# Performance work log

Hardware: AMD Instinct MI355X
Metric: run time of the kernel (lower is better)

## Reference

```python
import jax, jax.numpy as jnp
import numpy as np

B, C, H, W = 1, 128, 384, 512
MAX_DISP = 3  # 7x7 = 49 shifts


def setup_inputs() -> dict:
    key = jax.random.key(0)
    kx, ky = jax.random.split(key)
    x = jax.random.normal(kx, (B, C, H, W), dtype=jnp.float32)
    y = jax.random.normal(ky, (B, C, H, W), dtype=jnp.float32)
    return {"x": x, "y": y}


def reference(x, y):
    # out[j*7+i, h, w] = sum_{b,c} x[b,c,h,w] * y[b,c,h+(j-3), w+(i-3)]
    # with zero padding for out-of-range y (exactly the torch pad/slice math).
    b, c, h, w = x.shape
    yp = jnp.pad(y, ((0, 0), (0, 0), (MAX_DISP, MAX_DISP), (MAX_DISP, MAX_DISP)))
    outs = []
    for j in range(2 * MAX_DISP + 1):      # shiftY = j - 3
        for i in range(2 * MAX_DISP + 1):  # shiftX = i - 3
            # start (pad + shiftY, pad + shiftX) = (j, i)
            ysh = jax.lax.dynamic_slice(yp, (0, 0, j, i), (b, c, h, w))
            outs.append(jnp.sum(x * ysh, axis=(0, 1)))  # sum over batch AND channel
    out = jnp.stack(outs)           # [49, H, W]
    return out[None]                # [1, 49, H, W]
```

## Files before the change

### kernel.cpp

```cpp
#include <hip/hip_runtime.h>
#include <stdint.h>


typedef __attribute__((ext_vector_type(8))) short short8;
typedef __attribute__((ext_vector_type(4))) float floatx4;

constexpr int C = 128;
constexpr int H = 384;
constexpr int W = 512;
constexpr int HW = H * W;

constexpr int NROW = 10;
constexpr int NCOL = 40;
constexpr int KP   = 40;
constexpr int ROWB = NCOL * KP * 2;
constexpr int BUFE = NROW * NCOL * KP;
constexpr int NUNIT = NROW * 4 * (NCOL / 2);

__device__ __forceinline__ uint32_t pkbf(float a, float b) {
  uint32_t ua = (__float_as_uint(a) + 0x8000u) >> 16;
  uint32_t ub = (__float_as_uint(b) + 0x8000u) & 0xffff0000u;
  return ua | ub;
}

union S8U { uint32_t u[4]; short8 s; };

__device__ __forceinline__ void stage_unit(const float* __restrict__ y,
                                           uint16_t* __restrict__ buf,
                                           int kc, int h0, int ws_blk, int u) {
  const int c2  = u % 20;
  const int kb  = (u / 20) & 3;
  const int row = u / 80;
  const int r_abs = h0 - 3 + row;
  const int cb    = ws_blk - 4 + 2 * c2;
  const bool val = (r_abs >= 0) & (r_abs < H) & (cb >= 0) & (cb <= W - 2);
  const int r  = r_abs < 0 ? 0 : (r_abs >= H ? H - 1 : r_abs);
  const int cc = cb < 0 ? 0 : (cb > W - 2 ? W - 2 : cb);
  const float* src = y + (size_t)(kc * 32 + kb * 8) * HW + (size_t)r * W + cc;
  float2 f[8];
#pragma unroll
  for (int e = 0; e < 8; ++e)
    f[e] = *reinterpret_cast<const float2*>(src + (size_t)e * HW);
  uint4 v0, v1;
  v0.x = pkbf(f[0].x, f[1].x); v0.y = pkbf(f[2].x, f[3].x);
  v0.z = pkbf(f[4].x, f[5].x); v0.w = pkbf(f[6].x, f[7].x);
  v1.x = pkbf(f[0].y, f[1].y); v1.y = pkbf(f[2].y, f[3].y);
  v1.z = pkbf(f[4].y, f[5].y); v1.w = pkbf(f[6].y, f[7].y);
  if (!val) { v0 = make_uint4(0, 0, 0, 0); v1 = make_uint4(0, 0, 0, 0); }
  const int kbs  = kb ^ ((c2 >> 2) & 3);
  const int ldso = (row * NCOL + 2 * c2) * KP + kbs * 8;
  *reinterpret_cast<uint4*>(&buf[ldso])      = v0;
  *reinterpret_cast<uint4*>(&buf[ldso + KP]) = v1;
}

__global__ __launch_bounds__(512, 4)
void corr_mfma(const float* __restrict__ x, const float* __restrict__ y,
               float* __restrict__ out) {
  __shared__ uint16_t ys[BUFE];

  const int bid  = blockIdx.x;
  const int xcd  = bid & 7;
  const int idx  = bid >> 3;
  const int hg   = xcd * 12 + (idx >> 4);
  const int slab = idx & 15;
  const int h0     = hg * 4;
  const int ws_blk = slab * 32;
  const int tid  = threadIdx.x;
  const int wv   = tid >> 6;
  const int lane = tid & 63;
  const int m  = lane & 15;
  const int g  = lane >> 4;
  const int dh = wv >> 1;
  const int ww = wv & 1;
  const int h  = h0 + dh;
  const int ws = ws_blk + ww * 16;

  const bool has2 = (tid < NUNIT - 512);

  floatx4 acc[7][2];
#pragma unroll
  for (int j = 0; j < 7; ++j) {
    acc[j][0] = (floatx4){0.f, 0.f, 0.f, 0.f};
    acc[j][1] = (floatx4){0.f, 0.f, 0.f, 0.f};
  }

  const int col0 = ww * 16 + m + 1;
  int col1 = col0 + 16;
  if (col1 > NCOL - 1) col1 = NCOL - 1;
  const int fb0 = col0 * (KP * 2) + (g ^ ((col0 >> 3) & 3)) * 16;
  const int fb1 = col1 * (KP * 2) + (g ^ ((col1 >> 3) & 3)) * 16;

  const float* xb = x + (size_t)(g * 8) * HW + (size_t)h * W + (ws + m);

#pragma unroll
  for (int kc = 0; kc < 4; ++kc) {
    if (kc) __syncthreads();
    stage_unit(y, ys, kc, h0, ws_blk, tid);
    if (has2) stage_unit(y, ys, kc, h0, ws_blk, 512 + tid);

    short8 af;
    {
      float f[8];
#pragma unroll
      for (int e = 0; e < 8; ++e)
        f[e] = xb[(size_t)(kc * 32 + e) * HW];
      S8U s;
      s.u[0] = pkbf(f[0], f[1]);
      s.u[1] = pkbf(f[2], f[3]);
      s.u[2] = pkbf(f[4], f[5]);
      s.u[3] = pkbf(f[6], f[7]);
      af = s.s;
    }
    __syncthreads();

#pragma unroll
    for (int j = 0; j < 7; ++j) {
      const uint8_t* rb =
          reinterpret_cast<const uint8_t*>(ys) + (dh + j) * ROWB;
      const short8 b0 = *reinterpret_cast<const short8*>(rb + fb0);
      const short8 b1 = *reinterpret_cast<const short8*>(rb + fb1);
      acc[j][0] = __builtin_amdgcn_mfma_f32_16x16x32_bf16(af, b0, acc[j][0], 0, 0, 0);
      acc[j][1] = __builtin_amdgcn_mfma_f32_16x16x32_bf16(af, b1, acc[j][1], 0, 0, 0);
    }
  }

  __syncthreads();
  float* slabp = reinterpret_cast<float*>(ys) + wv * 544;
#pragma unroll
  for (int j = 0; j < 7; ++j) {
#pragma unroll
    for (int q = 0; q < 4; ++q) {
      slabp[(g * 4 + q) * 34 + m]      = acc[j][0][q];
      slabp[(g * 4 + q) * 34 + 16 + m] = acc[j][1][q];
    }
    const float vo0 = slabp[m * 34 + m + g];
    const float vo1 = slabp[m * 34 + m + g + 4];
    float* ob = out + (size_t)(j * 7 + g) * HW + (size_t)h * W + (ws + m);
    *ob = vo0;
    if (g < 3) ob[(size_t)4 * HW] = vo1;
  }
}

extern "C" void kernel_launch(void* const* d_in, const int* in_sizes, int n_in,
                              void* d_out, int out_size, void* d_ws, size_t ws_size,
                              hipStream_t stream) {
  const float* x = (const float*)d_in[0];
  const float* y = (const float*)d_in[1];
  float* out = (float*)d_out;
  corr_mfma<<<dim3(96 * 16), dim3(512), 0, stream>>>(x, y, out);
}
```

Measured before the change: 59.07 us.

## Halve block width and split vertical shifts across waves for more blocks

Each block now covers a 16-column tile instead of 32. The two waves per output row now split the seven vertical shift rows between them (4 and 3) instead of splitting columns. The grid doubles, per-block LDS shrinks, and launch bounds ask for 6 blocks per CU, all to raise occupancy and parallelism. The cost is a larger halo fraction (24 staged columns per 16 outputs), so y loads and bf16 conversions are duplicated more and x is loaded twice per row.

```diff
diff --git a/kernel.cpp b/kernel.cpp
--- a/kernel.cpp
+++ b/kernel.cpp
@@ -11,7 +11,7 @@
 constexpr int HW = H * W;
 
 constexpr int NROW = 10;
-constexpr int NCOL = 40;
+constexpr int NCOL = 24;
 constexpr int KP   = 40;
 constexpr int ROWB = NCOL * KP * 2;
 constexpr int BUFE = NROW * NCOL * KP;
@@ -28,9 +28,9 @@
 __device__ __forceinline__ void stage_unit(const float* __restrict__ y,
                                            uint16_t* __restrict__ buf,
                                            int kc, int h0, int ws_blk, int u) {
-  const int c2  = u % 20;
-  const int kb  = (u / 20) & 3;
-  const int row = u / 80;
+  const int c2  = u % 12;
+  const int kb  = (u / 12) & 3;
+  const int row = u / 48;
   const int r_abs = h0 - 3 + row;
   const int cb    = ws_blk - 4 + 2 * c2;
   const bool val = (r_abs >= 0) & (r_abs < H) & (cb >= 0) & (cb <= W - 2);
@@ -53,7 +53,7 @@
   *reinterpret_cast<uint4*>(&buf[ldso + KP]) = v1;
 }
 
-__global__ __launch_bounds__(512, 4)
+__global__ __launch_bounds__(512, 6)
 void corr_mfma(const float* __restrict__ x, const float* __restrict__ y,
                float* __restrict__ out) {
   __shared__ uint16_t ys[BUFE];
@@ -61,30 +61,32 @@
   const int bid  = blockIdx.x;
   const int xcd  = bid & 7;
   const int idx  = bid >> 3;
-  const int hg   = xcd * 12 + (idx >> 4);
-  const int slab = idx & 15;
+  const int hg   = xcd * 12 + (idx >> 5);
+  const int slab = idx & 31;
   const int h0     = hg * 4;
-  const int ws_blk = slab * 32;
+  const int ws_blk = slab * 16;
   const int tid  = threadIdx.x;
   const int wv   = tid >> 6;
   const int lane = tid & 63;
   const int m  = lane & 15;
   const int g  = lane >> 4;
   const int dh = wv >> 1;
-  const int ww = wv & 1;
+  const int kg = wv & 1;
   const int h  = h0 + dh;
-  const int ws = ws_blk + ww * 16;
+  const int ws = ws_blk;
+  const int j0 = kg ? 4 : 0;
+  const int nj = kg ? 3 : 4;
 
-  const bool has2 = (tid < NUNIT - 512);
+  const bool stg = (tid < NUNIT);
 
-  floatx4 acc[7][2];
+  floatx4 acc[4][2];
 #pragma unroll
-  for (int j = 0; j < 7; ++j) {
-    acc[j][0] = (floatx4){0.f, 0.f, 0.f, 0.f};
-    acc[j][1] = (floatx4){0.f, 0.f, 0.f, 0.f};
+  for (int jj = 0; jj < 4; ++jj) {
+    acc[jj][0] = (floatx4){0.f, 0.f, 0.f, 0.f};
+    acc[jj][1] = (floatx4){0.f, 0.f, 0.f, 0.f};
   }
 
-  const int col0 = ww * 16 + m + 1;
+  const int col0 = m + 1;
   int col1 = col0 + 16;
   if (col1 > NCOL - 1) col1 = NCOL - 1;
   const int fb0 = col0 * (KP * 2) + (g ^ ((col0 >> 3) & 3)) * 16;
@@ -95,8 +97,7 @@
 #pragma unroll
   for (int kc = 0; kc < 4; ++kc) {
     if (kc) __syncthreads();
-    stage_unit(y, ys, kc, h0, ws_blk, tid);
-    if (has2) stage_unit(y, ys, kc, h0, ws_blk, 512 + tid);
+    if (stg) stage_unit(y, ys, kc, h0, ws_blk, tid);
 
     short8 af;
     {
@@ -114,30 +115,36 @@
     __syncthreads();
 
 #pragma unroll
-    for (int j = 0; j < 7; ++j) {
-      const uint8_t* rb =
-          reinterpret_cast<const uint8_t*>(ys) + (dh + j) * ROWB;
-      const short8 b0 = *reinterpret_cast<const short8*>(rb + fb0);
-      const short8 b1 = *reinterpret_cast<const short8*>(rb + fb1);
-      acc[j][0] = __builtin_amdgcn_mfma_f32_16x16x32_bf16(af, b0, acc[j][0], 0, 0, 0);
-      acc[j][1] = __builtin_amdgcn_mfma_f32_16x16x32_bf16(af, b1, acc[j][1], 0, 0, 0);
+    for (int jj = 0; jj < 4; ++jj) {
+      if (jj < nj) {
+        const int j = j0 + jj;
+        const uint8_t* rb =
+            reinterpret_cast<const uint8_t*>(ys) + (dh + j) * ROWB;
+        const short8 b0 = *reinterpret_cast<const short8*>(rb + fb0);
+        const short8 b1 = *reinterpret_cast<const short8*>(rb + fb1);
+        acc[jj][0] = __builtin_amdgcn_mfma_f32_16x16x32_bf16(af, b0, acc[jj][0], 0, 0, 0);
+        acc[jj][1] = __builtin_amdgcn_mfma_f32_16x16x32_bf16(af, b1, acc[jj][1], 0, 0, 0);
+      }
     }
   }
 
   __syncthreads();
   float* slabp = reinterpret_cast<float*>(ys) + wv * 544;
 #pragma unroll
-  for (int j = 0; j < 7; ++j) {
+  for (int jj = 0; jj < 4; ++jj) {
+    if (jj < nj) {
+      const int j = j0 + jj;
 #pragma unroll
-    for (int q = 0; q < 4; ++q) {
-      slabp[(g * 4 + q) * 34 + m]      = acc[j][0][q];
-      slabp[(g * 4 + q) * 34 + 16 + m] = acc[j][1][q];
+      for (int q = 0; q < 4; ++q) {
+        slabp[(g * 4 + q) * 34 + m]      = acc[jj][0][q];
+        slabp[(g * 4 + q) * 34 + 16 + m] = acc[jj][1][q];
+      }
+      const float vo0 = slabp[m * 34 + m + g];
+      const float vo1 = slabp[m * 34 + m + g + 4];
+      float* ob = out + (size_t)(j * 7 + g) * HW + (size_t)h * W + (ws + m);
+      *ob = vo0;
+      if (g < 3) ob[(size_t)4 * HW] = vo1;
     }
-    const float vo0 = slabp[m * 34 + m + g];
-    const float vo1 = slabp[m * 34 + m + g + 4];
-    float* ob = out + (size_t)(j * 7 + g) * HW + (size_t)h * W + (ws + m);
-    *ob = vo0;
-    if (g < 3) ob[(size_t)4 * HW] = vo1;
   }
 }
 
@@ -147,5 +154,5 @@
   const float* x = (const float*)d_in[0];
   const float* y = (const float*)d_in[1];
   float* out = (float*)d_out;
-  corr_mfma<<<dim3(96 * 16), dim3(512), 0, stream>>>(x, y, out);
+  corr_mfma<<<dim3(96 * 32), dim3(512), 0, stream>>>(x, y, out);
 }
```

Result: slower. 63.47 us (+7.5%).

## Double-buffer LDS staging and prefetch next channel chunk during MFMA

Applied to the files above, without the earlier changes.

Splits the shared y tile into two buffers and issues the global loads for the next 32-channel chunk (y and x) before running the MFMAs on the current one. The converted values are written into the other buffer afterward, so one barrier per chunk remains. This aims to hide global-load latency behind matrix work, but it doubles LDS use to about 64 KB per block, which likely cuts resident blocks per CU. The overflow staging units are still loaded synchronously.

```diff
diff --git a/kernel.cpp b/kernel.cpp
--- a/kernel.cpp
+++ b/kernel.cpp
@@ -25,38 +25,52 @@
 
 union S8U { uint32_t u[4]; short8 s; };
 
-__device__ __forceinline__ void stage_unit(const float* __restrict__ y,
-                                           uint16_t* __restrict__ buf,
-                                           int kc, int h0, int ws_blk, int u) {
+__device__ __forceinline__ void unit_decode(const float* __restrict__ y,
+                                            int kc, int h0, int ws_blk, int u,
+                                            const float*& src, bool& val,
+                                            int& ldso) {
   const int c2  = u % 20;
   const int kb  = (u / 20) & 3;
   const int row = u / 80;
   const int r_abs = h0 - 3 + row;
   const int cb    = ws_blk - 4 + 2 * c2;
-  const bool val = (r_abs >= 0) & (r_abs < H) & (cb >= 0) & (cb <= W - 2);
+  val = (r_abs >= 0) & (r_abs < H) & (cb >= 0) & (cb <= W - 2);
   const int r  = r_abs < 0 ? 0 : (r_abs >= H ? H - 1 : r_abs);
   const int cc = cb < 0 ? 0 : (cb > W - 2 ? W - 2 : cb);
-  const float* src = y + (size_t)(kc * 32 + kb * 8) * HW + (size_t)r * W + cc;
-  float2 f[8];
-#pragma unroll
-  for (int e = 0; e < 8; ++e)
-    f[e] = *reinterpret_cast<const float2*>(src + (size_t)e * HW);
+  src = y + (size_t)(kc * 32 + kb * 8) * HW + (size_t)r * W + cc;
+  const int kbs = kb ^ ((c2 >> 2) & 3);
+  ldso = (row * NCOL + 2 * c2) * KP + kbs * 8;
+}
+
+__device__ __forceinline__ void unit_store(uint16_t* __restrict__ buf,
+                                           const float2 f[8], bool val,
+                                           int ldso) {
   uint4 v0, v1;
   v0.x = pkbf(f[0].x, f[1].x); v0.y = pkbf(f[2].x, f[3].x);
   v0.z = pkbf(f[4].x, f[5].x); v0.w = pkbf(f[6].x, f[7].x);
   v1.x = pkbf(f[0].y, f[1].y); v1.y = pkbf(f[2].y, f[3].y);
   v1.z = pkbf(f[4].y, f[5].y); v1.w = pkbf(f[6].y, f[7].y);
   if (!val) { v0 = make_uint4(0, 0, 0, 0); v1 = make_uint4(0, 0, 0, 0); }
-  const int kbs  = kb ^ ((c2 >> 2) & 3);
-  const int ldso = (row * NCOL + 2 * c2) * KP + kbs * 8;
   *reinterpret_cast<uint4*>(&buf[ldso])      = v0;
   *reinterpret_cast<uint4*>(&buf[ldso + KP]) = v1;
+}
+
+__device__ __forceinline__ void stage_plain(const float* __restrict__ y,
+                                            uint16_t* __restrict__ buf,
+                                            int kc, int h0, int ws_blk, int u) {
+  const float* src; bool val; int ldso;
+  unit_decode(y, kc, h0, ws_blk, u, src, val, ldso);
+  float2 f[8];
+#pragma unroll
+  for (int e = 0; e < 8; ++e)
+    f[e] = *reinterpret_cast<const float2*>(src + (size_t)e * HW);
+  unit_store(buf, f, val, ldso);
 }
 
 __global__ __launch_bounds__(512, 4)
 void corr_mfma(const float* __restrict__ x, const float* __restrict__ y,
                float* __restrict__ out) {
-  __shared__ uint16_t ys[BUFE];
+  __shared__ uint16_t ys[2][BUFE];
 
   const int bid  = blockIdx.x;
   const int xcd  = bid & 7;
@@ -92,40 +106,64 @@
 
   const float* xb = x + (size_t)(g * 8) * HW + (size_t)h * W + (ws + m);
 
+  stage_plain(y, ys[0], 0, h0, ws_blk, tid);
+  if (has2) stage_plain(y, ys[0], 0, h0, ws_blk, 512 + tid);
+  short8 af_cur;
+  {
+    float f[8];
+#pragma unroll
+    for (int e = 0; e < 8; ++e) f[e] = xb[(size_t)e * HW];
+    S8U s;
+    s.u[0] = pkbf(f[0], f[1]);
+    s.u[1] = pkbf(f[2], f[3]);
+    s.u[2] = pkbf(f[4], f[5]);
+    s.u[3] = pkbf(f[6], f[7]);
+    af_cur = s.s;
+  }
+  __syncthreads();
+
 #pragma unroll
   for (int kc = 0; kc < 4; ++kc) {
-    if (kc) __syncthreads();
-    stage_unit(y, ys, kc, h0, ws_blk, tid);
-    if (has2) stage_unit(y, ys, kc, h0, ws_blk, 512 + tid);
-
-    short8 af;
-    {
-      float f[8];
+    float2 F[8];
+    float axf[8];
+    bool v = false; int o = 0;
+    if (kc < 3) {
+      const float* s1;
+      unit_decode(y, kc + 1, h0, ws_blk, tid, s1, v, o);
 #pragma unroll
       for (int e = 0; e < 8; ++e)
-        f[e] = xb[(size_t)(kc * 32 + e) * HW];
-      S8U s;
-      s.u[0] = pkbf(f[0], f[1]);
-      s.u[1] = pkbf(f[2], f[3]);
-      s.u[2] = pkbf(f[4], f[5]);
-      s.u[3] = pkbf(f[6], f[7]);
-      af = s.s;
+        F[e] = *reinterpret_cast<const float2*>(s1 + (size_t)e * HW);
+#pragma unroll
+      for (int e = 0; e < 8; ++e)
+        axf[e] = xb[(size_t)((kc + 1) * 32 + e) * HW];
     }
-    __syncthreads();
 
+    const uint16_t* buf = ys[kc & 1];
 #pragma unroll
     for (int j = 0; j < 7; ++j) {
       const uint8_t* rb =
-          reinterpret_cast<const uint8_t*>(ys) + (dh + j) * ROWB;
+          reinterpret_cast<const uint8_t*>(buf) + (dh + j) * ROWB;
       const short8 b0 = *reinterpret_cast<const short8*>(rb + fb0);
       const short8 b1 = *reinterpret_cast<const short8*>(rb + fb1);
-      acc[j][0] = __builtin_amdgcn_mfma_f32_16x16x32_bf16(af, b0, acc[j][0], 0, 0, 0);
-      acc[j][1] = __builtin_amdgcn_mfma_f32_16x16x32_bf16(af, b1, acc[j][1], 0, 0, 0);
+      acc[j][0] = __builtin_amdgcn_mfma_f32_16x16x32_bf16(af_cur, b0, acc[j][0], 0, 0, 0);
+      acc[j][1] = __builtin_amdgcn_mfma_f32_16x16x32_bf16(af_cur, b1, acc[j][1], 0, 0, 0);
     }
+
+    if (kc < 3) {
+      uint16_t* nbuf = ys[(kc + 1) & 1];
+      unit_store(nbuf, F, v, o);
+      if (has2) stage_plain(y, nbuf, kc + 1, h0, ws_blk, 512 + tid);
+      S8U s;
+      s.u[0] = pkbf(axf[0], axf[1]);
+      s.u[1] = pkbf(axf[2], axf[3]);
+      s.u[2] = pkbf(axf[4], axf[5]);
+      s.u[3] = pkbf(axf[6], axf[7]);
+      af_cur = s.s;
+    }
+    __syncthreads();
   }
 
-  __syncthreads();
-  float* slabp = reinterpret_cast<float*>(ys) + wv * 544;
+  float* slabp = reinterpret_cast<float*>(&ys[0][0]) + wv * 544;
 #pragma unroll
   for (int j = 0; j < 7; ++j) {
 #pragma unroll
```

Result: faster. 55.01 us, median of 2 (-6.9%).
